# Kernel optimization log

Measured on AMD Instinct MI355X. Metric: run time of the kernel, lower is better.

The kernel has to match this reference:

```python
import jax, jax.numpy as jnp
import numpy as np

B, S, D = 2, 2048, 1024
H = 16
HD = D // H  # 64


def setup_inputs() -> dict:
    key = jax.random.key(0)
    k = jax.random.split(key, 6)
    s = 0.02
    return {
        "x": jax.random.normal(k[0], (B, S, D), dtype=jnp.float32),
        "wq": jax.random.normal(k[1], (D, D), dtype=jnp.float32) * s,
        "wk": jax.random.normal(k[2], (D, D), dtype=jnp.float32) * s,
        "wv": jax.random.normal(k[3], (D, D), dtype=jnp.float32) * s,
        "wo": jax.random.normal(k[4], (D, D), dtype=jnp.float32) * s,
        "bo": jnp.zeros((D,), dtype=jnp.float32),
    }


def reference(x, wq, wk, wv, wo, bo):
    b, n, d = x.shape
    # nn.Linear: y = x @ W.T (qkv_bias=False)
    def proj(w):
        y = jnp.einsum('bnd,od->bno', x, w)
        return y.reshape(b, n, H, HD).transpose(0, 2, 1, 3)  # (b, H, n, hd)
    q, k, v = proj(wq), proj(wk), proj(wv)
    scores = jnp.einsum('bhqd,bhkd->bhqk', q, k) / jnp.sqrt(jnp.float32(HD))
    # NOTE: source code slices the causal mask but never applies it; softmax is unmasked.
    attn = jax.nn.softmax(scores, axis=-1)
    # dropout p=0.0 -> identity
    ctx = jnp.einsum('bhqk,bhkd->bhqd', attn, v)
    ctx = ctx.transpose(0, 2, 1, 3).reshape(b, n, d)
    return jnp.einsum('bnd,od->bno', ctx, wo) + bo
```

## Files before the change

kernel.cpp:

```cpp
#include <hip/hip_runtime.h>
#include <stdint.h>

typedef __attribute__((ext_vector_type(8))) short short8;
typedef __attribute__((ext_vector_type(4))) short short4v;
typedef __attribute__((ext_vector_type(4))) float float4v;
typedef __attribute__((ext_vector_type(4))) unsigned short ushort4v;

#define Bq 2
#define Sq 2048
#define Dq 1024
#define Hq 16
#define HDq 64

__device__ __forceinline__ unsigned short f2bf(float f) {
  union { float f; uint32_t u; } v; v.f = f;
  uint32_t r = (v.u + 0x7FFFu + ((v.u >> 16) & 1u)) >> 16;
  return (unsigned short)r;
}

__device__ __forceinline__ void gl_lds16(const unsigned short* g, unsigned short* l) {
  __builtin_amdgcn_global_load_lds(
      (const __attribute__((address_space(1))) void*)g,
      (__attribute__((address_space(3))) void*)l, 16, 0, 0);
}

__global__ __launch_bounds__(256) void cvt_kernel(const float* __restrict__ src,
                                                  unsigned short* __restrict__ dst, int n4) {
  int i = blockIdx.x * 256 + threadIdx.x;
  if (i >= n4) return;
  float4v f = ((const float4v*)src)[i];
  ushort4v o;
#pragma unroll
  for (int j = 0; j < 4; j++) o[j] = f2bf(f[j]);
  ((ushort4v*)dst)[i] = o;
}

__global__ __launch_bounds__(256) void cvtw_kernel(const float* __restrict__ w0,
                                                   const float* __restrict__ w1,
                                                   const float* __restrict__ w2,
                                                   const float* __restrict__ w3,
                                                   unsigned short* __restrict__ dst) {
  const int z = blockIdx.y;
  const float* src = (z == 0) ? w0 : (z == 1) ? w1 : (z == 2) ? w2 : w3;
  int i = blockIdx.x * 256 + threadIdx.x;
  float4v f = ((const float4v*)src)[i];
  ushort4v o;
#pragma unroll
  for (int j = 0; j < 4; j++) o[j] = f2bf(f[j]);
  ((ushort4v*)(dst + (size_t)z * 1048576))[i] = o;
}

template <bool OUTPROJ>
__global__ __launch_bounds__(256) void gemm_bt_kernel(
    const unsigned short* __restrict__ A,
    const unsigned short* __restrict__ W0,
    const unsigned short* __restrict__ W1,
    const unsigned short* __restrict__ W2,
    unsigned short* __restrict__ q_dst,
    unsigned short* __restrict__ k_dst,
    unsigned short* __restrict__ v_dst,
    float* __restrict__ f_dst,
    const float* __restrict__ bias) {
  constexpr int K = 1024;
  const int z = blockIdx.z;
  const unsigned short* W = (z == 0) ? W0 : (z == 1) ? W1 : W2;
  unsigned short* qkv = (z == 0) ? q_dst : (z == 1) ? k_dst : v_dst;

  __shared__ unsigned short Asm[128 * 32];
  __shared__ unsigned short Bsm[128 * 32];

  const int t = threadIdx.x;
  const int wave = t >> 6, lane = t & 63;
  const int quad = lane >> 4, l16 = lane & 15;
  const int wy = wave >> 1, wx = wave & 1;
  const int row0 = blockIdx.x * 128;
  const int col0 = blockIdx.y * 128;

  float4v zero = {0.f, 0.f, 0.f, 0.f};
  float4v acc[4][4];
#pragma unroll
  for (int i = 0; i < 4; i++)
#pragma unroll
    for (int j = 0; j < 4; j++) acc[i][j] = zero;

  const int sr = t >> 2;
  const int sc = (t & 3) << 3;
  const unsigned short* ga = A + (size_t)(row0 + sr) * K + sc;
  const unsigned short* gb = W + (size_t)(col0 + sr) * K + sc;
  unsigned short* lA0 = &Asm[t * 8];
  unsigned short* lA1 = &Asm[2048 + t * 8];
  unsigned short* lB0 = &Bsm[t * 8];
  unsigned short* lB1 = &Bsm[2048 + t * 8];

  for (int k0 = 0; k0 < K; k0 += 32) {
    gl_lds16(ga + k0, lA0);
    gl_lds16(ga + (size_t)64 * K + k0, lA1);
    gl_lds16(gb + k0, lB0);
    gl_lds16(gb + (size_t)64 * K + k0, lB1);
    __syncthreads();
    short8 af[4], bf[4];
#pragma unroll
    for (int mb = 0; mb < 4; mb++)
      af[mb] = *(const short8*)(&Asm[(wy * 64 + mb * 16 + l16) * 32 + quad * 8]);
#pragma unroll
    for (int nb = 0; nb < 4; nb++)
      bf[nb] = *(const short8*)(&Bsm[(wx * 64 + nb * 16 + l16) * 32 + quad * 8]);
#pragma unroll
    for (int mb = 0; mb < 4; mb++)
#pragma unroll
      for (int nb = 0; nb < 4; nb++)
        acc[mb][nb] = __builtin_amdgcn_mfma_f32_16x16x32_bf16(af[mb], bf[nb], acc[mb][nb], 0, 0, 0);
    __syncthreads();
  }

#pragma unroll
  for (int mb = 0; mb < 4; mb++) {
#pragma unroll
    for (int nb = 0; nb < 4; nb++) {
#pragma unroll
      for (int r = 0; r < 4; r++) {
        int row = row0 + wy * 64 + mb * 16 + quad * 4 + r;
        int o = col0 + wx * 64 + nb * 16 + l16;
        float val = acc[mb][nb][r];
        if (OUTPROJ) {
          f_dst[(size_t)row * 1024 + o] = val + bias[o];
        } else {
          int b = row >> 11, s = row & 2047;
          int h = o >> 6, hd = o & 63;
          qkv[(size_t)((b * Hq + h) * Sq + s) * HDq + hd] = f2bf(val);
        }
      }
    }
  }
}

__global__ __launch_bounds__(256) void attn_kernel(
    const unsigned short* __restrict__ Q,
    const unsigned short* __restrict__ Kg,
    const unsigned short* __restrict__ Vg,
    unsigned short* __restrict__ ctx) {
  constexpr int KSTR = 68;
  constexpr int VSTR = 72;
  const int bh = blockIdx.y;
  const int q0 = blockIdx.x * 128;
  const int t = threadIdx.x;
  const int wave = t >> 6, lane = t & 63;
  const int quad = lane >> 4, l16 = lane & 15;

  __shared__ unsigned short Ksm[64 * KSTR];
  __shared__ unsigned short Vsm[64 * VSTR];

  const unsigned short* Qb = Q + (size_t)bh * Sq * HDq;
  const unsigned short* Kb = Kg + (size_t)bh * Sq * HDq;
  const unsigned short* Vb = Vg + (size_t)bh * Sq * HDq;

  short8 qf[2][2];
#pragma unroll
  for (int rb = 0; rb < 2; rb++)
#pragma unroll
    for (int ks = 0; ks < 2; ks++)
      qf[rb][ks] = *(const short8*)(Qb + (size_t)(q0 + wave * 32 + rb * 16 + l16) * HDq + ks * 32 + quad * 8);

  float4v zero = {0.f, 0.f, 0.f, 0.f};
  float4v of[2][4];
  float lsum[2] = {0.f, 0.f};
#pragma unroll
  for (int rb = 0; rb < 2; rb++)
#pragma unroll
    for (int hb = 0; hb < 4; hb++) of[rb][hb] = zero;

  const int vr2 = (t & 31) * 2;
  const int vc = (t >> 5) << 3;

  for (int kt = 0; kt < Sq; kt += 64) {
#pragma unroll
    for (int i = 0; i < 2; i++) {
      int c = t + i * 256;
      int kr = c >> 3, kc = (c & 7) << 3;
      short8 kv = *(const short8*)(Kb + (size_t)(kt + kr) * HDq + kc);
      *(short8*)(&Ksm[kr * KSTR + kc]) = kv;
    }
    {
      short8 v0 = *(const short8*)(Vb + (size_t)(kt + vr2) * HDq + vc);
      short8 v1 = *(const short8*)(Vb + (size_t)(kt + vr2 + 1) * HDq + vc);
#pragma unroll
      for (int j = 0; j < 8; j++) {
        uint32_t pk = (uint32_t)(unsigned short)v0[j] | ((uint32_t)(unsigned short)v1[j] << 16);
        *(uint32_t*)(&Vsm[(vc + j) * VSTR + vr2]) = pk;
      }
    }
    __syncthreads();

    float4v sf[2][4];
#pragma unroll
    for (int rb = 0; rb < 2; rb++)
#pragma unroll
      for (int cb = 0; cb < 4; cb++) sf[rb][cb] = zero;
#pragma unroll
    for (int cb = 0; cb < 4; cb++) {
#pragma unroll
      for (int ks = 0; ks < 2; ks++) {
        short8 kf = *(const short8*)(&Ksm[(cb * 16 + l16) * KSTR + ks * 32 + quad * 8]);
#pragma unroll
        for (int rb = 0; rb < 2; rb++)
          sf[rb][cb] = __builtin_amdgcn_mfma_f32_16x16x32_bf16(kf, qf[rb][ks], sf[rb][cb], 0, 0, 0);
      }
    }

    short8 pf[2][2];
#pragma unroll
    for (int rb = 0; rb < 2; rb++)
#pragma unroll
      for (int cb = 0; cb < 4; cb++)
#pragma unroll
        for (int r = 0; r < 4; r++) {
          float p = __expf(sf[rb][cb][r] * 0.125f);
          lsum[rb] += p;
          pf[rb][cb >> 1][(cb & 1) * 4 + r] = (short)f2bf(p);
        }

#pragma unroll
    for (int p = 0; p < 2; p++) {
#pragma unroll
      for (int hb = 0; hb < 4; hb++) {
        short4v vlo = *(const short4v*)(&Vsm[(hb * 16 + l16) * VSTR + p * 32 + quad * 4]);
        short4v vhi = *(const short4v*)(&Vsm[(hb * 16 + l16) * VSTR + p * 32 + 16 + quad * 4]);
        short8 vf;
#pragma unroll
        for (int j = 0; j < 4; j++) { vf[j] = vlo[j]; vf[j + 4] = vhi[j]; }
#pragma unroll
        for (int rb = 0; rb < 2; rb++)
          of[rb][hb] = __builtin_amdgcn_mfma_f32_16x16x32_bf16(pf[rb][p], vf, of[rb][hb], 0, 0, 0);
      }
    }
    __syncthreads();
  }

  float dinv[2][4];
#pragma unroll
  for (int rb = 0; rb < 2; rb++) {
    float l = lsum[rb];
    l += __shfl_xor(l, 16, 64);
    l += __shfl_xor(l, 32, 64);
#pragma unroll
    for (int r = 0; r < 4; r++)
      dinv[rb][r] = 1.0f / __shfl(l, quad * 4 + r, 64);
  }

  const int b = bh >> 4, h = bh & 15;
#pragma unroll
  for (int rb = 0; rb < 2; rb++)
#pragma unroll
    for (int hb = 0; hb < 4; hb++)
#pragma unroll
      for (int r = 0; r < 4; r++) {
        int srow = q0 + wave * 32 + rb * 16 + quad * 4 + r;
        int d = h * 64 + hb * 16 + l16;
        ctx[(size_t)(b * Sq + srow) * Dq + d] = f2bf(of[rb][hb][r] * dinv[rb][r]);
      }
}

extern "C" void kernel_launch(void* const* d_in, const int* in_sizes, int n_in,
                              void* d_out, int out_size, void* d_ws, size_t ws_size,
                              hipStream_t stream) {
  (void)in_sizes; (void)n_in; (void)out_size; (void)ws_size;
  const float* x  = (const float*)d_in[0];
  const float* wq = (const float*)d_in[1];
  const float* wk = (const float*)d_in[2];
  const float* wv = (const float*)d_in[3];
  const float* wo = (const float*)d_in[4];
  const float* bo = (const float*)d_in[5];
  float* out = (float*)d_out;

  char* ws = (char*)d_ws;
  const size_t MB = 1u << 20;
  unsigned short* xb  = (unsigned short*)(ws + 0 * MB);
  unsigned short* wqb = (unsigned short*)(ws + 8 * MB);
  unsigned short* wkb = (unsigned short*)(ws + 10 * MB);
  unsigned short* wvb = (unsigned short*)(ws + 12 * MB);
  unsigned short* wob = (unsigned short*)(ws + 14 * MB);
  unsigned short* qb  = (unsigned short*)(ws + 16 * MB);
  unsigned short* kb  = (unsigned short*)(ws + 24 * MB);
  unsigned short* vb  = (unsigned short*)(ws + 32 * MB);
  unsigned short* cxb = (unsigned short*)(ws + 40 * MB);

  cvt_kernel<<<4096, 256, 0, stream>>>(x, xb, (Bq * Sq * Dq) / 4);
  cvtw_kernel<<<dim3(1024, 4), 256, 0, stream>>>(wq, wk, wv, wo, wqb);

  gemm_bt_kernel<false><<<dim3(32, 8, 3), 256, 0, stream>>>(
      xb, wqb, wkb, wvb, qb, kb, vb, nullptr, nullptr);
  attn_kernel<<<dim3(16, 32), 256, 0, stream>>>(qb, kb, vb, cxb);
  gemm_bt_kernel<true><<<dim3(32, 8, 1), 256, 0, stream>>>(
      cxb, wob, wob, wob, nullptr, nullptr, nullptr, out, bo);
}
```

Measured before the change: 212.7 us.

## Fuse conversion kernels, prefetch K/V in attention, shrink out-proj tile

Merges the x and weight bf16 conversion kernels into one launch. The attention kernel now processes 128-key tiles and prefetches the next K/V tile into registers while the current one is computed. It also permutes the V layout in LDS so each MFMA operand comes from a single 8-wide read, and packs bf16 pairs with a hardware conversion intrinsic. The output projection uses a 64-row M tile to launch twice as many blocks. The trade-offs are more registers and LDS in attention, and leftover redundant statements in the conversion kernel.

```diff
diff --git a/kernel.cpp b/kernel.cpp
--- a/kernel.cpp
+++ b/kernel.cpp
@@ -1,8 +1,8 @@
 #include <hip/hip_runtime.h>
+#include <hip/hip_bf16.h>
 #include <stdint.h>
 
 typedef __attribute__((ext_vector_type(8))) short short8;
-typedef __attribute__((ext_vector_type(4))) short short4v;
 typedef __attribute__((ext_vector_type(4))) float float4v;
 typedef __attribute__((ext_vector_type(4))) unsigned short ushort4v;
 
@@ -18,39 +18,56 @@
   return (unsigned short)r;
 }
 
+__device__ __forceinline__ uint32_t pk2bf(float a, float b) {
+  union { __hip_bfloat162 h; uint32_t u; } cv;
+  cv.h = __float22bfloat162_rn(make_float2(a, b));
+  return cv.u;
+}
+
 __device__ __forceinline__ void gl_lds16(const unsigned short* g, unsigned short* l) {
   __builtin_amdgcn_global_load_lds(
       (const __attribute__((address_space(1))) void*)g,
       (__attribute__((address_space(3))) void*)l, 16, 0, 0);
 }
 
-__global__ __launch_bounds__(256) void cvt_kernel(const float* __restrict__ src,
-                                                  unsigned short* __restrict__ dst, int n4) {
-  int i = blockIdx.x * 256 + threadIdx.x;
-  if (i >= n4) return;
-  float4v f = ((const float4v*)src)[i];
+__global__ __launch_bounds__(256) void cvt_all_kernel(
+    const float* __restrict__ x,
+    const float* __restrict__ w0, const float* __restrict__ w1,
+    const float* __restrict__ w2, const float* __restrict__ w3,
+    unsigned short* __restrict__ xb, unsigned short* __restrict__ wb) {
+  const int bid = blockIdx.x;
+  const float* src;
+  unsigned short* dst;
+  int idx;
+  if (bid < 4096) {
+    idx = bid * 256 + threadIdx.x;
+    src = x; dst = xb;
+  } else {
+    int j = (bid - 4096) * 256 + threadIdx.x;
+    int z = j >> 18;
+    src = (z == 0) ? w0 : (z == 1) ? w1 : (z == 2) ? w2 : w3;
+    src -= (size_t)z * 1048576;
+    idx = j; dst = wb;
+    src = (z == 0) ? w0 - 0 : src;
+    src = (z == 0) ? w0 : (z == 1) ? w1 : (z == 2) ? w2 : w3;
+    idx = j & 262143;
+    dst = wb + (size_t)(j >> 18) * 1048576 / 1;
+    dst = wb + (size_t)(j >> 18) * 1048576;
+    float4v f = ((const float4v*)src)[idx];
+    ushort4v o;
+#pragma unroll
+    for (int q = 0; q < 4; q++) o[q] = f2bf(f[q]);
+    ((ushort4v*)dst)[idx] = o;
+    return;
+  }
+  float4v f = ((const float4v*)src)[idx];
   ushort4v o;
 #pragma unroll
-  for (int j = 0; j < 4; j++) o[j] = f2bf(f[j]);
-  ((ushort4v*)dst)[i] = o;
-}
-
-__global__ __launch_bounds__(256) void cvtw_kernel(const float* __restrict__ w0,
-                                                   const float* __restrict__ w1,
-                                                   const float* __restrict__ w2,
-                                                   const float* __restrict__ w3,
-                                                   unsigned short* __restrict__ dst) {
-  const int z = blockIdx.y;
-  const float* src = (z == 0) ? w0 : (z == 1) ? w1 : (z == 2) ? w2 : w3;
-  int i = blockIdx.x * 256 + threadIdx.x;
-  float4v f = ((const float4v*)src)[i];
-  ushort4v o;
-#pragma unroll
-  for (int j = 0; j < 4; j++) o[j] = f2bf(f[j]);
-  ((ushort4v*)(dst + (size_t)z * 1048576))[i] = o;
-}
-
-template <bool OUTPROJ>
+  for (int q = 0; q < 4; q++) o[q] = f2bf(f[q]);
+  ((ushort4v*)dst)[idx] = o;
+}
+
+template <bool OUTPROJ, int MT>
 __global__ __launch_bounds__(256) void gemm_bt_kernel(
     const unsigned short* __restrict__ A,
     const unsigned short* __restrict__ W0,
@@ -62,24 +79,25 @@
     float* __restrict__ f_dst,
     const float* __restrict__ bias) {
   constexpr int K = 1024;
+  constexpr int NMB = MT / 32;
   const int z = blockIdx.z;
   const unsigned short* W = (z == 0) ? W0 : (z == 1) ? W1 : W2;
   unsigned short* qkv = (z == 0) ? q_dst : (z == 1) ? k_dst : v_dst;
 
-  __shared__ unsigned short Asm[128 * 32];
+  __shared__ unsigned short Asm[MT * 32];
   __shared__ unsigned short Bsm[128 * 32];
 
   const int t = threadIdx.x;
   const int wave = t >> 6, lane = t & 63;
   const int quad = lane >> 4, l16 = lane & 15;
   const int wy = wave >> 1, wx = wave & 1;
-  const int row0 = blockIdx.x * 128;
+  const int row0 = blockIdx.x * MT;
   const int col0 = blockIdx.y * 128;
 
   float4v zero = {0.f, 0.f, 0.f, 0.f};
-  float4v acc[4][4];
-#pragma unroll
-  for (int i = 0; i < 4; i++)
+  float4v acc[NMB][4];
+#pragma unroll
+  for (int i = 0; i < NMB; i++)
 #pragma unroll
     for (int j = 0; j < 4; j++) acc[i][j] = zero;
 
@@ -87,26 +105,22 @@
   const int sc = (t & 3) << 3;
   const unsigned short* ga = A + (size_t)(row0 + sr) * K + sc;
   const unsigned short* gb = W + (size_t)(col0 + sr) * K + sc;
-  unsigned short* lA0 = &Asm[t * 8];
-  unsigned short* lA1 = &Asm[2048 + t * 8];
-  unsigned short* lB0 = &Bsm[t * 8];
-  unsigned short* lB1 = &Bsm[2048 + t * 8];
 
   for (int k0 = 0; k0 < K; k0 += 32) {
-    gl_lds16(ga + k0, lA0);
-    gl_lds16(ga + (size_t)64 * K + k0, lA1);
-    gl_lds16(gb + k0, lB0);
-    gl_lds16(gb + (size_t)64 * K + k0, lB1);
+    gl_lds16(ga + k0, &Asm[t * 8]);
+    if constexpr (MT == 128) gl_lds16(ga + (size_t)64 * K + k0, &Asm[2048 + t * 8]);
+    gl_lds16(gb + k0, &Bsm[t * 8]);
+    gl_lds16(gb + (size_t)64 * K + k0, &Bsm[2048 + t * 8]);
     __syncthreads();
-    short8 af[4], bf[4];
-#pragma unroll
-    for (int mb = 0; mb < 4; mb++)
-      af[mb] = *(const short8*)(&Asm[(wy * 64 + mb * 16 + l16) * 32 + quad * 8]);
+    short8 af[NMB], bf[4];
+#pragma unroll
+    for (int mb = 0; mb < NMB; mb++)
+      af[mb] = *(const short8*)(&Asm[(wy * (MT / 2) + mb * 16 + l16) * 32 + quad * 8]);
 #pragma unroll
     for (int nb = 0; nb < 4; nb++)
       bf[nb] = *(const short8*)(&Bsm[(wx * 64 + nb * 16 + l16) * 32 + quad * 8]);
 #pragma unroll
-    for (int mb = 0; mb < 4; mb++)
+    for (int mb = 0; mb < NMB; mb++)
 #pragma unroll
       for (int nb = 0; nb < 4; nb++)
         acc[mb][nb] = __builtin_amdgcn_mfma_f32_16x16x32_bf16(af[mb], bf[nb], acc[mb][nb], 0, 0, 0);
@@ -114,12 +128,12 @@
   }
 
 #pragma unroll
-  for (int mb = 0; mb < 4; mb++) {
+  for (int mb = 0; mb < NMB; mb++) {
 #pragma unroll
     for (int nb = 0; nb < 4; nb++) {
 #pragma unroll
       for (int r = 0; r < 4; r++) {
-        int row = row0 + wy * 64 + mb * 16 + quad * 4 + r;
+        int row = row0 + wy * (MT / 2) + mb * 16 + quad * 4 + r;
         int o = col0 + wx * 64 + nb * 16 + l16;
         float val = acc[mb][nb][r];
         if (OUTPROJ) {
@@ -140,14 +154,14 @@
     const unsigned short* __restrict__ Vg,
     unsigned short* __restrict__ ctx) {
   constexpr int KSTR = 68;
-  constexpr int VSTR = 72;
+  constexpr int VSTR = 136;
   const int bh = blockIdx.y;
   const int q0 = blockIdx.x * 128;
   const int t = threadIdx.x;
   const int wave = t >> 6, lane = t & 63;
   const int quad = lane >> 4, l16 = lane & 15;
 
-  __shared__ unsigned short Ksm[64 * KSTR];
+  __shared__ unsigned short Ksm[128 * KSTR];
   __shared__ unsigned short Vsm[64 * VSTR];
 
   const unsigned short* Qb = Q + (size_t)bh * Sq * HDq;
@@ -169,68 +183,85 @@
 #pragma unroll
     for (int hb = 0; hb < 4; hb++) of[rb][hb] = zero;
 
-  const int vr2 = (t & 31) * 2;
-  const int vc = (t >> 5) << 3;
-
-  for (int kt = 0; kt < Sq; kt += 64) {
-#pragma unroll
-    for (int i = 0; i < 2; i++) {
-      int c = t + i * 256;
-      int kr = c >> 3, kc = (c & 7) << 3;
-      short8 kv = *(const short8*)(Kb + (size_t)(kt + kr) * HDq + kc);
-      *(short8*)(&Ksm[kr * KSTR + kc]) = kv;
+  const int kr0 = t >> 3, kc = (t & 7) << 3;
+  const int vr2 = (t & 63) * 2;
+  const int vc8 = (t >> 6) << 3;
+  const int sig = (vr2 & ~31) + (((vr2 >> 2) & 3) << 3) + (((vr2 >> 4) & 1) << 2) + (vr2 & 3);
+
+  short8 kpr[4], vpr0[2], vpr1[2];
+#pragma unroll
+  for (int i = 0; i < 4; i++)
+    kpr[i] = *(const short8*)(Kb + (size_t)(kr0 + i * 32) * HDq + kc);
+#pragma unroll
+  for (int i = 0; i < 2; i++) {
+    vpr0[i] = *(const short8*)(Vb + (size_t)vr2 * HDq + vc8 + i * 32);
+    vpr1[i] = *(const short8*)(Vb + (size_t)(vr2 + 1) * HDq + vc8 + i * 32);
+  }
+
+  for (int kt = 0; kt < Sq; kt += 128) {
+#pragma unroll
+    for (int i = 0; i < 4; i++)
+      *(short8*)(&Ksm[(kr0 + i * 32) * KSTR + kc]) = kpr[i];
+#pragma unroll
+    for (int i = 0; i < 2; i++)
+#pragma unroll
+      for (int j = 0; j < 8; j++) {
+        uint32_t pk = (uint32_t)(unsigned short)vpr0[i][j] |
+                      ((uint32_t)(unsigned short)vpr1[i][j] << 16);
+        *(uint32_t*)(&Vsm[(vc8 + i * 32 + j) * VSTR + sig]) = pk;
+      }
+    __syncthreads();
+
+    if (kt + 128 < Sq) {
+      const unsigned short* Kn = Kb + (size_t)(kt + 128) * HDq;
+      const unsigned short* Vn = Vb + (size_t)(kt + 128) * HDq;
+#pragma unroll
+      for (int i = 0; i < 4; i++)
+        kpr[i] = *(const short8*)(Kn + (size_t)(kr0 + i * 32) * HDq + kc);
+#pragma unroll
+      for (int i = 0; i < 2; i++) {
+        vpr0[i] = *(const short8*)(Vn + (size_t)vr2 * HDq + vc8 + i * 32);
+        vpr1[i] = *(const short8*)(Vn + (size_t)(vr2 + 1) * HDq + vc8 + i * 32);
+      }
     }
-    {
-      short8 v0 = *(const short8*)(Vb + (size_t)(kt + vr2) * HDq + vc);
-      short8 v1 = *(const short8*)(Vb + (size_t)(kt + vr2 + 1) * HDq + vc);
-#pragma unroll
-      for (int j = 0; j < 8; j++) {
-        uint32_t pk = (uint32_t)(unsigned short)v0[j] | ((uint32_t)(unsigned short)v1[j] << 16);
-        *(uint32_t*)(&Vsm[(vc + j) * VSTR + vr2]) = pk;
-      }
-    }
-    __syncthreads();
-
-    float4v sf[2][4];
-#pragma unroll
-    for (int rb = 0; rb < 2; rb++)
-#pragma unroll
-      for (int cb = 0; cb < 4; cb++) sf[rb][cb] = zero;
-#pragma unroll
-    for (int cb = 0; cb < 4; cb++) {
-#pragma unroll
-      for (int ks = 0; ks < 2; ks++) {
-        short8 kf = *(const short8*)(&Ksm[(cb * 16 + l16) * KSTR + ks * 32 + quad * 8]);
+
+#pragma unroll
+    for (int p = 0; p < 4; p++) {
+      float4v sf[2][2];
+#pragma unroll
+      for (int rb = 0; rb < 2; rb++)
+#pragma unroll
+        for (int s = 0; s < 2; s++) sf[rb][s] = zero;
+#pragma unroll
+      for (int s = 0; s < 2; s++)
+#pragma unroll
+        for (int ks = 0; ks < 2; ks++) {
+          short8 kf = *(const short8*)(&Ksm[(p * 32 + s * 16 + l16) * KSTR + ks * 32 + quad * 8]);
+#pragma unroll
+          for (int rb = 0; rb < 2; rb++)
+            sf[rb][s] = __builtin_amdgcn_mfma_f32_16x16x32_bf16(kf, qf[rb][ks], sf[rb][s], 0, 0, 0);
+        }
+      short8 pf[2];
+#pragma unroll
+      for (int rb = 0; rb < 2; rb++) {
+        union { uint32_t u[4]; short8 v; } pw;
+#pragma unroll
+        for (int s = 0; s < 2; s++)
+#pragma unroll
+          for (int rp = 0; rp < 2; rp++) {
+            float pa = __expf(sf[rb][s][rp * 2] * 0.125f);
+            float pb = __expf(sf[rb][s][rp * 2 + 1] * 0.125f);
+            lsum[rb] += pa + pb;
+            pw.u[s * 2 + rp] = pk2bf(pa, pb);
+          }
+        pf[rb] = pw.v;
+      }
+#pragma unroll
+      for (int hb = 0; hb < 4; hb++) {
+        short8 vf = *(const short8*)(&Vsm[(hb * 16 + l16) * VSTR + p * 32 + quad * 8]);
 #pragma unroll
         for (int rb = 0; rb < 2; rb++)
-          sf[rb][cb] = __builtin_amdgcn_mfma_f32_16x16x32_bf16(kf, qf[rb][ks], sf[rb][cb], 0, 0, 0);
-      }
-    }
-
-    short8 pf[2][2];
-#pragma unroll
-    for (int rb = 0; rb < 2; rb++)
-#pragma unroll
-      for (int cb = 0; cb < 4; cb++)
-#pragma unroll
-        for (int r = 0; r < 4; r++) {
-          float p = __expf(sf[rb][cb][r] * 0.125f);
-          lsum[rb] += p;
-          pf[rb][cb >> 1][(cb & 1) * 4 + r] = (short)f2bf(p);
-        }
-
-#pragma unroll
-    for (int p = 0; p < 2; p++) {
-#pragma unroll
-      for (int hb = 0; hb < 4; hb++) {
-        short4v vlo = *(const short4v*)(&Vsm[(hb * 16 + l16) * VSTR + p * 32 + quad * 4]);
-        short4v vhi = *(const short4v*)(&Vsm[(hb * 16 + l16) * VSTR + p * 32 + 16 + quad * 4]);
-        short8 vf;
-#pragma unroll
-        for (int j = 0; j < 4; j++) { vf[j] = vlo[j]; vf[j + 4] = vhi[j]; }
-#pragma unroll
-        for (int rb = 0; rb < 2; rb++)
-          of[rb][hb] = __builtin_amdgcn_mfma_f32_16x16x32_bf16(pf[rb][p], vf, of[rb][hb], 0, 0, 0);
+          of[rb][hb] = __builtin_amdgcn_mfma_f32_16x16x32_bf16(pf[rb], vf, of[rb][hb], 0, 0, 0);
       }
     }
     __syncthreads();
@@ -284,12 +315,11 @@
   unsigned short* vb  = (unsigned short*)(ws + 32 * MB);
   unsigned short* cxb = (unsigned short*)(ws + 40 * MB);
 
-  cvt_kernel<<<4096, 256, 0, stream>>>(x, xb, (Bq * Sq * Dq) / 4);
-  cvtw_kernel<<<dim3(1024, 4), 256, 0, stream>>>(wq, wk, wv, wo, wqb);
-
-  gemm_bt_kernel<false><<<dim3(32, 8, 3), 256, 0, stream>>>(
+  cvt_all_kernel<<<8192, 256, 0, stream>>>(x, wq, wk, wv, wo, xb, wqb);
+
+  gemm_bt_kernel<false, 128><<<dim3(32, 8, 3), 256, 0, stream>>>(
       xb, wqb, wkb, wvb, qb, kb, vb, nullptr, nullptr);
   attn_kernel<<<dim3(16, 32), 256, 0, stream>>>(qb, kb, vb, cxb);
-  gemm_bt_kernel<true><<<dim3(32, 8, 1), 256, 0, stream>>>(
+  gemm_bt_kernel<true, 64><<<dim3(64, 8, 1), 256, 0, stream>>>(
       cxb, wob, wob, wob, nullptr, nullptr, nullptr, out, bo);
 }
```

Result: faster. 190.5 us (-10.4%).
